# Optimization experiments

Hardware: AMD Instinct MI355X
Metric: run time of the kernel (lower is better)

## Reference

```python
import jax, jax.numpy as jnp
import numpy as np

B, L, D, H, FF, K = 2, 2048, 1024, 16, 4096, 5
HD = D // H
EPS = 1e-5

def _rope_matrix():
    pos = jnp.arange(L, dtype=jnp.float32)
    inv = 1.0 / (10000.0 ** (jnp.arange(0, HD, 2, dtype=jnp.float32) / HD))
    ang = pos[:, None] * inv[None, :]                       # [L, HD//2]
    # buffer layout matches torch: cat([cos, sin], -1) -> [1,1,L,HD]
    return jnp.concatenate([jnp.cos(ang), jnp.sin(ang)], -1)[None, None]

def _alibi():
    i = jnp.arange(L)
    dist = jnp.clip(i[:, None] - i[None, :], 0, None).astype(jnp.float32)
    slopes = 2.0 ** (-(2.0 ** (-(np.log2(H) - 3.0))) * jnp.arange(H, dtype=jnp.float32))
    return slopes[:, None, None] * dist                     # [H,L,L]

def _apply_rope(x, pe):
    # faithful even/odd slicing of the concatenated [cos|sin] buffer
    xe, xo = x[..., ::2], x[..., 1::2]
    c, s = pe[..., ::2], pe[..., 1::2]
    return jnp.concatenate([xe * c - xo * s, xe * s + xo * c], -1)

def _ln(x, g, b):
    m = x.mean(-1, keepdims=True)
    v = ((x - m) ** 2).mean(-1, keepdims=True)
    return (x - m) * jax.lax.rsqrt(v + EPS) * g + b

def _attn(x, wq, bq, wk, bk, wv, bv, wo, bo, pe, alibi):
    q = (x @ wq + bq).reshape(B, L, H, HD).transpose(0, 2, 1, 3)
    k = (x @ wk + bk).reshape(B, L, H, HD).transpose(0, 2, 1, 3)
    v = (x @ wv + bv).reshape(B, L, H, HD).transpose(0, 2, 1, 3)
    q = _apply_rope(q, pe)
    k = _apply_rope(k, pe)
    scores = jnp.einsum('bhqd,bhkd->bhqk', q, k) * (HD ** -0.5) + alibi[None]
    w = jax.nn.softmax(scores, axis=-1)
    o = jnp.einsum('bhqk,bhkd->bhqd', w, v).transpose(0, 2, 1, 3).reshape(B, L, D)
    return o @ wo + bo

def _conv_block(x, g, b, pw1_w, pw1_b, dw_w, dw_b, bn_g, bn_b, pw2_w, pw2_b):
    res = x
    h = _ln(x, g, b)
    h = h @ pw1_w + pw1_b                                   # pointwise 1: [B,L,2D]
    h = h[..., :D] * jax.nn.sigmoid(h[..., D:])             # GLU -> [B,L,D]
    h = h.transpose(0, 2, 1)                                # [B,D,L]
    w = dw_w[:, None, ::-1]                                 # ConvTranspose1d(stride=1,pad=K//2) == corr with flipped kernel
    h = jax.lax.conv_general_dilated(h, w, (1,), [(K // 2, K // 2)],
        dimension_numbers=('NCH', 'OIH', 'NCH'), feature_group_count=D)
    h = h + dw_b[None, :, None]
    h = h * jax.lax.rsqrt(jnp.float32(1.0 + EPS)) * bn_g[None, :, None] + bn_b[None, :, None]  # eval BN
    h = h * jax.nn.relu6(h + 3.0) / 6.0                     # hardswish
    h = h.transpose(0, 2, 1) @ pw2_w + pw2_b                # pointwise 2: [B,L,D]
    return h + res[:, :1, :]                                # Upsample(size=1) residual (nearest -> t=0)

def reference(memory, wq, bq, wk, bk, wv, bv, wo, bo, n1_g, n1_b,
              cln_g, cln_b, pw1_w, pw1_b, dw_w, dw_b, bn_g, bn_b, pw2_w, pw2_b,
              proj_w, proj_b, proj2_w, proj2_b, lin1_w, lin1_b, lin2_w, lin2_b,
              n3_g, n3_b):
    pe = _rope_matrix()
    alibi = _alibi()
    tgt2 = _attn(memory, wq, bq, wk, bk, wv, bv, wo, bo, pe, alibi)
    memory = memory + _ln(tgt2, n1_g, n1_b)
    conv = _conv_block(memory, cln_g, cln_b, pw1_w, pw1_b, dw_w, dw_b,
                       bn_g, bn_b, pw2_w, pw2_b)
    proj = jnp.einsum('bld,lm->bmd', memory, proj_w) + proj_b[:, None]   # Linear over seq axis
    proj = proj @ proj2_w + proj2_b
    memory = proj + conv
    tgt2 = jax.nn.gelu(memory @ lin1_w + lin1_b, approximate=False) @ lin2_w + lin2_b
    return _ln(memory + tgt2, n3_g, n3_b)

def setup_inputs():
    ks = iter(jax.random.split(jax.random.key(0), 48))
    def w(shape, s=0.02):
        return jax.random.normal(next(ks), shape, dtype=jnp.float32) * s
    z = lambda *s: jnp.zeros(s, dtype=jnp.float32)
    o = lambda *s: jnp.ones(s, dtype=jnp.float32)
    return {
        'memory': jax.random.normal(next(ks), (B, L, D), dtype=jnp.float32),
        'wq': w((D, D)), 'bq': z(D), 'wk': w((D, D)), 'bk': z(D),
        'wv': w((D, D)), 'bv': z(D), 'wo': w((D, D)), 'bo': z(D),
        'n1_g': o(D), 'n1_b': z(D),
        'cln_g': o(D), 'cln_b': z(D),
        'pw1_w': w((D, 2 * D)), 'pw1_b': z(2 * D),
        'dw_w': w((D, K), 0.1), 'dw_b': z(D),
        'bn_g': o(D), 'bn_b': z(D),
        'pw2_w': w((D, D)), 'pw2_b': z(D),
        'proj_w': w((L, L)), 'proj_b': z(L),
        'proj2_w': w((D, D)), 'proj2_b': z(D),
        'lin1_w': w((D, FF)), 'lin1_b': z(FF),
        'lin2_w': w((FF, D)), 'lin2_b': z(D),
        'n3_g': o(D), 'n3_b': z(D),
    }
```

## Files before the change

### kernel.cpp

```cpp
#include <hip/hip_runtime.h>
#include <hip/hip_bf16.h>
#include <math.h>

constexpr int Bc = 2, Lc = 2048, Dc = 1024, Hc = 16, HDc = 64, FFc = 4096;
constexpr int NT = Bc * Lc;
constexpr size_t TD = (size_t)NT * Dc;
constexpr size_t MEG = 1024 * 1024;

__device__ __forceinline__ float ldf(const float* p) { return *p; }
__device__ __forceinline__ unsigned short f2b(float f) {
  __hip_bfloat16 h = __float2bfloat16(f);
  return *reinterpret_cast<unsigned short*>(&h);
}

using frag   = __attribute__((ext_vector_type(8))) short;
using f32x4v = __attribute__((ext_vector_type(4))) float;

__device__ __forceinline__ void async16(const unsigned short* g, unsigned short* l) {
  __builtin_amdgcn_global_load_lds(
      (const __attribute__((address_space(1))) unsigned int*)g,
      (__attribute__((address_space(3))) unsigned int*)l, 16, 0, 0);
}

__device__ __forceinline__ float block_sum(float v, float* red) {
  const int lane = threadIdx.x & 63, w = threadIdx.x >> 6;
  #pragma unroll
  for (int o = 32; o > 0; o >>= 1) v += __shfl_down(v, o, 64);
  __syncthreads();
  if (lane == 0) red[w] = v;
  __syncthreads();
  return red[0] + red[1] + red[2] + red[3];
}

__global__ __launch_bounds__(256)
void convert_bf16_kernel(const float* __restrict__ IN, unsigned short* __restrict__ OUT)
{
  const size_t gid = (size_t)blockIdx.x * 256 + threadIdx.x;
  const float4 v = *(const float4*)(IN + gid * 4);
  ushort4 o;
  o.x = f2b(v.x); o.y = f2b(v.y); o.z = f2b(v.z); o.w = f2b(v.w);
  *(ushort4*)(OUT + gid * 4) = o;
}

__global__ __launch_bounds__(256)
void transpose_convert_kernel(const float* __restrict__ IN, unsigned short* __restrict__ OUT,
                              int R, int C, long long sIn, long long sOut)
{
  __shared__ float tile[64][65];
  const int t = threadIdx.x;
  const float* in = IN + (long long)blockIdx.z * sIn;
  unsigned short* out = OUT + (long long)blockIdx.z * sOut;
  const int r0 = blockIdx.y * 64, c0 = blockIdx.x * 64;
  #pragma unroll
  for (int i = 0; i < 4; i++) {
    const int r = (t >> 4) + i * 16, c4 = (t & 15) * 4;
    const float4 v = *(const float4*)(in + (size_t)(r0 + r) * C + c0 + c4);
    tile[r][c4+0] = v.x; tile[r][c4+1] = v.y; tile[r][c4+2] = v.z; tile[r][c4+3] = v.w;
  }
  __syncthreads();
  #pragma unroll
  for (int i = 0; i < 4; i++) {
    const int cc = (t >> 4) + i * 16, rr4 = (t & 15) * 4;
    ushort4 o;
    o.x = f2b(tile[rr4+0][cc]); o.y = f2b(tile[rr4+1][cc]);
    o.z = f2b(tile[rr4+2][cc]); o.w = f2b(tile[rr4+3][cc]);
    *(ushort4*)(out + (size_t)(c0 + cc) * R + r0 + rr4) = o;
  }
}

struct TPack {
  const float* in[10]; unsigned short* out[10];
  int R[10], C[10], tx[10], start[10];
};
__global__ __launch_bounds__(256)
void fused_transpose_kernel(TPack p)
{
  __shared__ float tile[64][65];
  const int bid = blockIdx.x;
  int s = 0;
  #pragma unroll
  for (int i = 1; i < 10; i++) s = (bid >= p.start[i]) ? i : s;
  const float* in = p.in[s];
  unsigned short* out = p.out[s];
  const int R = p.R[s], C = p.C[s];
  const int local = bid - p.start[s];
  const int bx = local % p.tx[s], by = local / p.tx[s];
  const int r0 = by * 64, c0 = bx * 64;
  const int t = threadIdx.x;
  #pragma unroll
  for (int i = 0; i < 4; i++) {
    const int r = (t >> 4) + i * 16, c4 = (t & 15) * 4;
    const float4 v = *(const float4*)(in + (size_t)(r0 + r) * C + c0 + c4);
    tile[r][c4+0] = v.x; tile[r][c4+1] = v.y; tile[r][c4+2] = v.z; tile[r][c4+3] = v.w;
  }
  __syncthreads();
  #pragma unroll
  for (int i = 0; i < 4; i++) {
    const int cc = (t >> 4) + i * 16, rr4 = (t & 15) * 4;
    ushort4 o;
    o.x = f2b(tile[rr4+0][cc]); o.y = f2b(tile[rr4+1][cc]);
    o.z = f2b(tile[rr4+2][cc]); o.w = f2b(tile[rr4+3][cc]);
    *(ushort4*)(out + (size_t)(c0 + cc) * R + r0 + rr4) = o;
  }
}

constexpr int EPI_BIAS = 0, EPI_BIAS_ROW = 1, EPI_GELU = 2, EPI_ADD = 3, EPI_ADDROW0 = 4,
              EPI_QKV = 5;

template<int BM, int EPI, bool OUTBF, bool OUTBOTH>
__global__ __launch_bounds__(256)
void mfma_gemm_kernel(const unsigned short* __restrict__ A, const unsigned short* __restrict__ Bt,
                      const float* __restrict__ bias, const float* __restrict__ bias2,
                      const float* __restrict__ bias3, const float* __restrict__ extra,
                      float* __restrict__ C, unsigned short* __restrict__ Cbf,
                      int M, int N, int K,
                      long long sA, long long sB, long long sC)
{
  constexpr int NTt = (BM == 128) ? 4 : 2;
  __shared__ unsigned short As[2][BM][4][8];
  __shared__ unsigned short Bs[2][128][4][8];
  const int tid = threadIdx.x;
  const int l = tid & 63, w = tid >> 6;
  const int wm = (BM == 128) ? (w & 1) * 64 : 0;
  const int wn = (BM == 128) ? (w >> 1) * 64 : w * 32;
  const int m0 = blockIdx.y * BM, n0 = blockIdx.x * 128;
  const unsigned short* Ap = A + (long long)blockIdx.z * sA;
  const unsigned short* Bp = Bt + (long long)blockIdx.z * sB;

  f32x4v acc[4][NTt];
  #pragma unroll
  for (int mt = 0; mt < 4; mt++)
    #pragma unroll
    for (int nt = 0; nt < NTt; nt++) acc[mt][nt] = {0.f, 0.f, 0.f, 0.f};

  const int c_ = l >> 4, rm = l & 15;
  int rrB[2], ggB[2];
  #pragma unroll
  for (int j = 0; j < 2; j++) {
    const int chunk = w * 128 + j * 64 + l;
    rrB[j] = chunk >> 2;
    ggB[j] = (chunk & 3) ^ ((rrB[j] >> 1) & 3);
  }
  int rrA = 0, ggA = 0;
  if constexpr (BM == 64) {
    const int chunkA = w * 64 + l;
    rrA = chunkA >> 2;
    ggA = (chunkA & 3) ^ ((rrA >> 1) & 3);
  }

  auto stage = [&](int bi, int k0) {
    if constexpr (BM == 128) {
      #pragma unroll
      for (int j = 0; j < 2; j++) {
        async16(Ap + (size_t)(m0 + rrB[j]) * K + k0 + ggB[j] * 8,
                &As[bi][0][0][0] + (size_t)(w * 128 + j * 64) * 8);
        async16(Bp + (size_t)(n0 + rrB[j]) * K + k0 + ggB[j] * 8,
                &Bs[bi][0][0][0] + (size_t)(w * 128 + j * 64) * 8);
      }
    } else {
      async16(Ap + (size_t)(m0 + rrA) * K + k0 + ggA * 8,
              &As[bi][0][0][0] + (size_t)(w * 64) * 8);
      #pragma unroll
      for (int j = 0; j < 2; j++)
        async16(Bp + (size_t)(n0 + rrB[j]) * K + k0 + ggB[j] * 8,
                &Bs[bi][0][0][0] + (size_t)(w * 128 + j * 64) * 8);
    }
  };

  stage(0, 0);
  __syncthreads();
  int cur = 0;
  const int sg = (rm >> 1) & 3;

  for (int k0 = 0; k0 < K; k0 += 32) {
    if (k0 + 32 < K) stage(cur ^ 1, k0 + 32);

    frag af[4], bfr[NTt];
    #pragma unroll
    for (int mt = 0; mt < 4; mt++)
      af[mt] = *(const frag*)&As[cur][wm + mt * 16 + rm][c_ ^ sg][0];
    #pragma unroll
    for (int nt = 0; nt < NTt; nt++)
      bfr[nt] = *(const frag*)&Bs[cur][wn + nt * 16 + rm][c_ ^ sg][0];
    #pragma unroll
    for (int mt = 0; mt < 4; mt++)
      #pragma unroll
      for (int nt = 0; nt < NTt; nt++)
        acc[mt][nt] = __builtin_amdgcn_mfma_f32_16x16x32_bf16(af[mt], bfr[nt], acc[mt][nt], 0, 0, 0);

    __syncthreads();
    cur ^= 1;
  }

  float* Cp = C + (long long)blockIdx.z * sC;
  unsigned short* Cbp = Cbf + (long long)blockIdx.z * sC;
  #pragma unroll
  for (int mt = 0; mt < 4; mt++) {
    #pragma unroll
    for (int nt = 0; nt < NTt; nt++) {
      const int mq = m0 + wm + mt * 16 + c_ * 4;
      const int n  = n0 + wn + nt * 16 + rm;
      if constexpr (EPI == EPI_QKV) {
        const float* bp = (n < 1024) ? bias : ((n < 2048) ? bias2 : bias3);
        const float bv_ = ldf(bp + (n & 1023));
        const float r0 = acc[mt][nt][0] + bv_;
        const float r1 = acc[mt][nt][1] + bv_;
        const float r2 = acc[mt][nt][2] + bv_;
        const float r3 = acc[mt][nt][3] + bv_;
        if (n < 2048) {
          float* dst = Cp + (size_t)(n >> 10) * TD + (size_t)mq * Dc + (n & 1023);
          dst[0] = r0; dst[Dc] = r1; dst[2 * Dc] = r2; dst[3 * Dc] = r3;
        } else {
          ushort4 o;
          o.x = f2b(r0); o.y = f2b(r1); o.z = f2b(r2); o.w = f2b(r3);
          *(ushort4*)(Cbp + (size_t)(mq >> 11) * ((size_t)Lc * Dc)
                      + (size_t)(n - 2048) * Lc + (mq & (Lc - 1))) = o;
        }
      } else {
        #pragma unroll
        for (int i = 0; i < 4; i++) {
          const int m = mq + i;
          float r = acc[mt][nt][i];
          if constexpr (EPI == EPI_BIAS || EPI == EPI_GELU || EPI == EPI_ADD || EPI == EPI_ADDROW0)
            r += ldf(bias + n);
          if constexpr (EPI == EPI_BIAS_ROW) r += ldf(bias + m);
          if constexpr (EPI == EPI_GELU)
            r = 0.5f * r * (1.0f + erff(r * 0.70710678118654752f));
          if constexpr (EPI == EPI_ADD) r += extra[(size_t)m * N + n];
          if constexpr (EPI == EPI_ADDROW0) r += extra[(size_t)(m >> 11) * ((size_t)Lc * Dc) + n];
          if constexpr (OUTBOTH) { Cp[(size_t)m * N + n] = r; Cbp[(size_t)m * N + n] = f2b(r); }
          else if constexpr (OUTBF) Cbp[(size_t)m * N + n] = f2b(r);
          else                      Cp[(size_t)m * N + n] = r;
        }
      }
    }
  }
}

__global__ __launch_bounds__(256)
void pe_fill_kernel(float* __restrict__ pet)
{
  const int gid = blockIdx.x * 256 + threadIdx.x;
  const int l = gid >> 6, t = gid & 63;
  const int j = t & 31;
  const float wj = exp2f(-(float)j * (13.2877123795494f / 32.0f));
  const float ang = (float)l * wj;
  pet[gid] = (t < 32) ? cosf(ang) : sinf(ang);
}

__global__ __launch_bounds__(256)
void rope2_kernel(const float* __restrict__ Qi, const float* __restrict__ Ki,
                  const float* __restrict__ pet,
                  unsigned short* __restrict__ Qo, unsigned short* __restrict__ Ko)
{
  int gid = blockIdx.x * 256 + threadIdx.x;
  const int sel = gid >= NT * Hc;
  if (sel) gid -= NT * Hc;
  const float* X = sel ? Ki : Qi;
  unsigned short* O = sel ? Ko : Qo;
  const int h = gid & (Hc - 1);
  const int token = gid >> 4;
  const int l = token & (Lc - 1);
  const float* p = X + (size_t)token * Dc + h * HDc;
  unsigned short* po = O + (size_t)token * Dc + h * HDc;
  const float* pr = pet + l * 64;
  float x[64], out[64];
  #pragma unroll
  for (int i = 0; i < 16; i++) *(float4*)&x[4*i] = *(const float4*)&p[4*i];
  #pragma unroll
  for (int u = 0; u < 32; u++) {
    const int base = (u < 16) ? (2 * u) : (32 + 2 * (u - 16));
    const float c = pr[base], s = pr[base + 1];
    out[u]      = x[2*u] * c - x[2*u+1] * s;
    out[32 + u] = x[2*u] * s + x[2*u+1] * c;
  }
  #pragma unroll
  for (int i = 0; i < 16; i++) {
    ushort4 o;
    o.x = f2b(out[4*i+0]); o.y = f2b(out[4*i+1]);
    o.z = f2b(out[4*i+2]); o.w = f2b(out[4*i+3]);
    *(ushort4*)&po[4*i] = o;
  }
}

__global__ __launch_bounds__(256)
void flash_attn_mfma_kernel(const unsigned short* __restrict__ Q,
                            const unsigned short* __restrict__ K,
                            const unsigned short* __restrict__ VT,
                            unsigned short* __restrict__ O)
{
  __shared__ unsigned short Qs[64][8][8];
  __shared__ unsigned short Ks[64][8][8];
  __shared__ unsigned short Vt[64][8][8];
  __shared__ unsigned short Ps[64][72];
  const int tid = threadIdx.x;
  const int l = tid & 63, w = tid >> 6;
  const int lg = l >> 4, lm = l & 15;
  const int q0 = blockIdx.x * 64;
  const int bh = blockIdx.y;
  const int b = bh >> 4, h = bh & 15;
  const size_t rowbase = (size_t)b * Lc;
  const size_t vbase = (size_t)b * Lc * Dc;
  const int dbase = h * 64;
  const float sc1 = 0.125f * 1.44269504f;
  const float sl2 = exp2f(-0.5f * (float)h) * 1.44269504f;

  #pragma unroll
  for (int j = 0; j < 2; j++) {
    const int chunk = (w * 2 + j) * 64 + l;
    const int r = chunk >> 3, gsrc = (chunk & 7) ^ (r & 7);
    async16(Q + (rowbase + q0 + r) * Dc + dbase + gsrc * 8,
            &Qs[0][0][0] + (size_t)chunk * 8);
  }
  __syncthreads();
  frag qf[2];
  #pragma unroll
  for (int s = 0; s < 2; s++)
    qf[s] = *(const frag*)&Qs[w * 16 + lm][(s * 4 + lg) ^ (lm & 7)][0];

  float m_i = -3.0e38f, l_i = 0.f;
  f32x4v acc_o[4];
  #pragma unroll
  for (int dt = 0; dt < 4; dt++) acc_o[dt] = {0.f, 0.f, 0.f, 0.f};

  for (int k0 = 0; k0 < Lc; k0 += 64) {
    __syncthreads();
    #pragma unroll
    for (int j = 0; j < 2; j++) {
      const int chunk = (w * 2 + j) * 64 + l;
      const int r = chunk >> 3, gsrc = (chunk & 7) ^ (r & 7);
      async16(K + (rowbase + k0 + r) * Dc + dbase + gsrc * 8,
              &Ks[0][0][0] + (size_t)chunk * 8);
      async16(VT + vbase + (size_t)(dbase + r) * Lc + k0 + gsrc * 8,
              &Vt[0][0][0] + (size_t)chunk * 8);
    }
    __syncthreads();

    f32x4v st[4];
    #pragma unroll
    for (int kt = 0; kt < 4; kt++) st[kt] = {0.f, 0.f, 0.f, 0.f};
    __builtin_amdgcn_s_setprio(1);
    #pragma unroll
    for (int kt = 0; kt < 4; kt++) {
      #pragma unroll
      for (int s = 0; s < 2; s++) {
        frag kf = *(const frag*)&Ks[kt * 16 + lm][(s * 4 + lg) ^ (lm & 7)][0];
        st[kt] = __builtin_amdgcn_mfma_f32_16x16x32_bf16(kf, qf[s], st[kt], 0, 0, 0);
      }
    }
    __builtin_amdgcn_s_setprio(0);

    const float qg = (float)(q0 + w * 16 + lm);
    float sv[4][4], tmax = -3.0e38f;
    #pragma unroll
    for (int kt = 0; kt < 4; kt++)
      #pragma unroll
      for (int i = 0; i < 4; i++) {
        const float kg = (float)(k0 + kt * 16 + lg * 4 + i);
        const float v = st[kt][i] * sc1 + sl2 * fmaxf(qg - kg, 0.0f);
        sv[kt][i] = v; tmax = fmaxf(tmax, v);
      }
    tmax = fmaxf(tmax, __shfl_xor(tmax, 16, 64));
    tmax = fmaxf(tmax, __shfl_xor(tmax, 32, 64));
    if (__any(tmax > m_i)) {
      const float mnew = fmaxf(m_i, tmax);
      const float alpha = exp2f(m_i - mnew);
      m_i = mnew;
      l_i *= alpha;
      float aO[4];
      #pragma unroll
      for (int i = 0; i < 4; i++) aO[i] = __shfl(alpha, lg * 4 + i, 64);
      #pragma unroll
      for (int dt = 0; dt < 4; dt++)
        #pragma unroll
        for (int i = 0; i < 4; i++) acc_o[dt][i] *= aO[i];
    }
    float rsum = 0.f;
    const int qrow = w * 16 + lm;
    #pragma unroll
    for (int kt = 0; kt < 4; kt++) {
      const float p0 = exp2f(sv[kt][0] - m_i), p1 = exp2f(sv[kt][1] - m_i);
      const float p2 = exp2f(sv[kt][2] - m_i), p3 = exp2f(sv[kt][3] - m_i);
      rsum += (p0 + p1) + (p2 + p3);
      ushort4 pk4;
      pk4.x = f2b(p0); pk4.y = f2b(p1); pk4.z = f2b(p2); pk4.w = f2b(p3);
      *(ushort4*)&Ps[qrow][kt * 16 + lg * 4] = pk4;
    }
    rsum += __shfl_xor(rsum, 16, 64);
    rsum += __shfl_xor(rsum, 32, 64);
    l_i += rsum;

    __builtin_amdgcn_s_setprio(1);
    #pragma unroll
    for (int c = 0; c < 2; c++) {
      frag ap = *(const frag*)&Ps[w * 16 + lm][c * 32 + lg * 8];
      #pragma unroll
      for (int dt = 0; dt < 4; dt++) {
        frag bv = *(const frag*)&Vt[dt * 16 + lm][(c * 4 + lg) ^ (lm & 7)][0];
        acc_o[dt] = __builtin_amdgcn_mfma_f32_16x16x32_bf16(ap, bv, acc_o[dt], 0, 0, 0);
      }
    }
    __builtin_amdgcn_s_setprio(0);
  }

  float lO[4];
  #pragma unroll
  for (int i = 0; i < 4; i++) lO[i] = 1.0f / __shfl(l_i, lg * 4 + i, 64);
  #pragma unroll
  for (int dt = 0; dt < 4; dt++)
    #pragma unroll
    for (int i = 0; i < 4; i++)
      Ps[w * 16 + lg * 4 + i][dt * 16 + lm] = f2b(acc_o[dt][i] * lO[i]);
  __syncthreads();
  #pragma unroll
  for (int j = 0; j < 2; j++) {
    const int chunk = (w * 2 + j) * 64 + l;
    const int r = chunk >> 3, g = chunk & 7;
    alignas(16) unsigned short tmp[8];
    #pragma unroll
    for (int t = 0; t < 8; t++) tmp[t] = Ps[r][g * 8 + t];
    *(uint4*)(O + (rowbase + q0 + r) * Dc + dbase + g * 8) = *(uint4*)tmp;
  }
}

__global__ __launch_bounds__(256)
void ln_res_cln_kernel(const float* __restrict__ X, const float* __restrict__ RES,
                       const float* __restrict__ g1, const float* __restrict__ b1,
                       const float* __restrict__ g2, const float* __restrict__ b2,
                       float* __restrict__ OUT1, unsigned short* __restrict__ OUT2)
{
  __shared__ float red4[4];
  const int row = blockIdx.x, tid = threadIdx.x;
  const size_t base = (size_t)row * Dc + tid * 4;
  const float4 xv = *(const float4*)(X + base);
  float s = xv.x + xv.y + xv.z + xv.w;
  s = block_sum(s, red4);
  const float mean = s * (1.0f / Dc);
  const float d0 = xv.x-mean, d1 = xv.y-mean, d2 = xv.z-mean, d3 = xv.w-mean;
  float ss = d0*d0 + d1*d1 + d2*d2 + d3*d3;
  ss = block_sum(ss, red4);
  const float rstd = rsqrtf(ss * (1.0f / Dc) + 1e-5f);
  const int c = tid * 4;
  const float4 rv = *(const float4*)(RES + base);
  float y0 = rv.x + d0*rstd*ldf(g1+c+0) + ldf(b1+c+0);
  float y1 = rv.y + d1*rstd*ldf(g1+c+1) + ldf(b1+c+1);
  float y2 = rv.z + d2*rstd*ldf(g1+c+2) + ldf(b1+c+2);
  float y3 = rv.w + d3*rstd*ldf(g1+c+3) + ldf(b1+c+3);
  *(float4*)(OUT1 + base) = make_float4(y0, y1, y2, y3);
  float s2 = y0 + y1 + y2 + y3;
  s2 = block_sum(s2, red4);
  const float mean2 = s2 * (1.0f / Dc);
  const float e0 = y0-mean2, e1 = y1-mean2, e2 = y2-mean2, e3 = y3-mean2;
  float ss2 = e0*e0 + e1*e1 + e2*e2 + e3*e3;
  ss2 = block_sum(ss2, red4);
  const float rstd2 = rsqrtf(ss2 * (1.0f / Dc) + 1e-5f);
  ushort4 o;
  o.x = f2b(e0*rstd2*ldf(g2+c+0) + ldf(b2+c+0));
  o.y = f2b(e1*rstd2*ldf(g2+c+1) + ldf(b2+c+1));
  o.z = f2b(e2*rstd2*ldf(g2+c+2) + ldf(b2+c+2));
  o.w = f2b(e3*rstd2*ldf(g2+c+3) + ldf(b2+c+3));
  *(ushort4*)(OUT2 + base) = o;
}

__global__ __launch_bounds__(256)
void ln_sum_kernel(const float* __restrict__ X, const float* __restrict__ Y,
                   const float* __restrict__ g, const float* __restrict__ be,
                   float* __restrict__ OUT)
{
  __shared__ float red4[4];
  const int row = blockIdx.x, tid = threadIdx.x;
  const size_t base = (size_t)row * Dc + tid * 4;
  const float4 xv = *(const float4*)(X + base);
  const float4 yv = *(const float4*)(Y + base);
  const float x0 = xv.x+yv.x, x1 = xv.y+yv.y, x2 = xv.z+yv.z, x3 = xv.w+yv.w;
  float s = x0 + x1 + x2 + x3;
  s = block_sum(s, red4);
  const float mean = s * (1.0f / Dc);
  const float d0 = x0-mean, d1 = x1-mean, d2 = x2-mean, d3 = x3-mean;
  float ss = d0*d0 + d1*d1 + d2*d2 + d3*d3;
  ss = block_sum(ss, red4);
  const float rstd = rsqrtf(ss * (1.0f / Dc) + 1e-5f);
  const int c = tid * 4;
  float4 o;
  o.x = d0*rstd*ldf(g+c+0) + ldf(be+c+0);
  o.y = d1*rstd*ldf(g+c+1) + ldf(be+c+1);
  o.z = d2*rstd*ldf(g+c+2) + ldf(be+c+2);
  o.w = d3*rstd*ldf(g+c+3) + ldf(be+c+3);
  *(float4*)(OUT + base) = o;
}

__global__ __launch_bounds__(256)
void glu_kernel(const float* __restrict__ H1, float* __restrict__ HG)
{
  const int gid = blockIdx.x * 256 + threadIdx.x;
  const int t = gid >> 8;
  const int c4 = (gid & 255) * 4;
  const float* p = H1 + (size_t)t * (2 * Dc);
  const float4 a = *(const float4*)(p + c4);
  const float4 gg = *(const float4*)(p + Dc + c4);
  float4 o;
  o.x = a.x / (1.0f + expf(-gg.x));
  o.y = a.y / (1.0f + expf(-gg.y));
  o.z = a.z / (1.0f + expf(-gg.z));
  o.w = a.w / (1.0f + expf(-gg.w));
  *(float4*)(HG + (size_t)t * Dc + c4) = o;
}

__global__ __launch_bounds__(256)
void dwconv_bf16_kernel(const float* __restrict__ HG, const float* __restrict__ w,
                        const float* __restrict__ wb, const float* __restrict__ gn,
                        const float* __restrict__ bb, unsigned short* __restrict__ OUT)
{
  const int gid = blockIdx.x * 256 + threadIdx.x;
  const int d = gid & (Dc - 1);
  const int l = (gid >> 10) & (Lc - 1);
  const int b = gid >> 21;
  const size_t rowb = (size_t)b * Lc;
  float acc = ldf(wb + d);
  #pragma unroll
  for (int s = 0; s < 5; s++) {
    const int lp = l + 2 - s;
    if (lp >= 0 && lp < Lc)
      acc += ldf(w + d * 5 + s) * HG[((rowb + lp) << 10) + d];
  }
  const float rs = rsqrtf(1.0f + 1e-5f);
  const float t = acc * rs * ldf(gn + d) + ldf(bb + d);
  OUT[gid] = f2b(t * fminf(fmaxf(t + 3.0f, 0.0f), 6.0f) * (1.0f / 6.0f));
}

extern "C" void kernel_launch(void* const* d_in, const int* in_sizes, int n_in,
                              void* d_out, int out_size, void* d_ws, size_t ws_size,
                              hipStream_t stream) {
  (void)in_sizes; (void)n_in; (void)out_size; (void)ws_size;
  const float* mem    = (const float*)d_in[0];
  const float* wq     = (const float*)d_in[1];
  const float* bq     = (const float*)d_in[2];
  const float* wk     = (const float*)d_in[3];
  const float* bk     = (const float*)d_in[4];
  const float* wv     = (const float*)d_in[5];
  const float* bv     = (const float*)d_in[6];
  const float* wo     = (const float*)d_in[7];
  const float* bo     = (const float*)d_in[8];
  const float* n1g    = (const float*)d_in[9];
  const float* n1b    = (const float*)d_in[10];
  const float* clng   = (const float*)d_in[11];
  const float* clnb   = (const float*)d_in[12];
  const float* pw1w   = (const float*)d_in[13];
  const float* pw1b   = (const float*)d_in[14];
  const float* dww    = (const float*)d_in[15];
  const float* dwb    = (const float*)d_in[16];
  const float* bng    = (const float*)d_in[17];
  const float* bnb    = (const float*)d_in[18];
  const float* pw2w   = (const float*)d_in[19];
  const float* pw2b   = (const float*)d_in[20];
  const float* projw  = (const float*)d_in[21];
  const float* projb  = (const float*)d_in[22];
  const float* proj2w = (const float*)d_in[23];
  const float* proj2b = (const float*)d_in[24];
  const float* lin1w  = (const float*)d_in[25];
  const float* lin1b  = (const float*)d_in[26];
  const float* lin2w  = (const float*)d_in[27];
  const float* lin2b  = (const float*)d_in[28];
  const float* n3g    = (const float*)d_in[29];
  const float* n3b    = (const float*)d_in[30];
  float* out = (float*)d_out;

  char* base = (char*)d_ws;
  float* qb   = (float*)base;
  float* kb   = qb + TD;
  float* big1 = kb + TD;
  float* big2 = big1 + TD;
  float* ob   = big2 + TD;
  unsigned short* abf  = (unsigned short*)(base + 5 * TD * 4);
  unsigned short* qbf  = abf + TD;
  unsigned short* kbf  = qbf + TD;
  unsigned short* vtb  = kbf + TD;
  unsigned short* m1T  = vtb + TD;
  unsigned short* ffbbf= m1T + TD;
  unsigned short* wt   = ffbbf + 4 * TD;
  unsigned short* wqT    = wt;
  unsigned short* wkT    = wqT + MEG;
  unsigned short* wvT    = wkT + MEG;
  unsigned short* woT    = wvT + MEG;
  unsigned short* pw1T   = woT + MEG;
  unsigned short* pw2T   = pw1T + 2*MEG;
  unsigned short* proj2T = pw2T + MEG;
  unsigned short* projwT = proj2T + MEG;
  unsigned short* lin1T  = projwT + 4*MEG;
  unsigned short* lin2T  = lin1T + 4*MEG;
  float* pet = (float*)(lin2T + 4*MEG);

  const dim3 blk(256);
  const long long LD = (long long)Lc * Dc;

  TPack tp;
  const float* tin[10]  = {wq, wk, wv, wo, pw1w, pw2w, proj2w, projw, lin1w, lin2w};
  unsigned short* tout[10] = {wqT, wkT, wvT, woT, pw1T, pw2T, proj2T, projwT, lin1T, lin2T};
  const int tR[10] = {1024,1024,1024,1024,1024,1024,1024,2048,1024,4096};
  const int tC[10] = {1024,1024,1024,1024,2048,1024,1024,2048,4096,1024};
  int startAcc = 0;
  for (int i = 0; i < 10; i++) {
    tp.in[i] = tin[i]; tp.out[i] = tout[i];
    tp.R[i] = tR[i]; tp.C[i] = tC[i]; tp.tx[i] = tC[i] / 64;
    tp.start[i] = startAcc;
    startAcc += (tR[i] / 64) * (tC[i] / 64);
  }
  fused_transpose_kernel<<<dim3(startAcc), blk, 0, stream>>>(tp);
  pe_fill_kernel<<<dim3(Lc * 64 / 256), blk, 0, stream>>>(pet);

  convert_bf16_kernel<<<dim3((unsigned)(TD/1024)),blk,0,stream>>>(mem, abf);
  mfma_gemm_kernel<128,EPI_QKV,false,false><<<dim3(24,32,1),blk,0,stream>>>(
      abf, wqT, bq, bk, bv, nullptr, qb, vtb, NT, 3*Dc, Dc, 0, 0, 0);
  rope2_kernel<<<dim3(2*NT*Hc/256),blk,0,stream>>>(qb, kb, pet, qbf, kbf);
  flash_attn_mfma_kernel<<<dim3(Lc/64, Bc*Hc),blk,0,stream>>>(qbf,kbf,vtb,abf);
  mfma_gemm_kernel<64,EPI_BIAS,false,false><<<dim3(8,64,1),blk,0,stream>>>(
      abf,woT,bo,nullptr,nullptr,nullptr,qb,nullptr,NT,Dc,Dc,0,0,0);
  ln_res_cln_kernel<<<dim3(NT),blk,0,stream>>>(qb, mem, n1g, n1b, clng, clnb, kb, abf);

  mfma_gemm_kernel<128,EPI_BIAS,false,false><<<dim3(16,32,1),blk,0,stream>>>(
      abf,pw1T,pw1b,nullptr,nullptr,nullptr,big1,nullptr,NT,2*Dc,Dc,0,0,0);
  glu_kernel<<<dim3((unsigned)(TD/4/256)),blk,0,stream>>>(big1, ob);
  dwconv_bf16_kernel<<<dim3((unsigned)(TD/256)),blk,0,stream>>>(ob, dww, dwb, bng, bnb, abf);
  mfma_gemm_kernel<64,EPI_ADDROW0,false,false><<<dim3(8,64,1),blk,0,stream>>>(
      abf,pw2T,pw2b,nullptr,nullptr,kb,big2,nullptr,NT,Dc,Dc,0,0,0);

  transpose_convert_kernel<<<dim3(16,32,2),blk,0,stream>>>(kb, m1T, 2048, 1024, LD, LD);
  mfma_gemm_kernel<64,EPI_BIAS_ROW,true,false><<<dim3(8,32,2),blk,0,stream>>>(
      projwT,m1T,projb,nullptr,nullptr,nullptr,nullptr,abf,Lc,Dc,Lc,0,LD,LD);
  mfma_gemm_kernel<64,EPI_ADD,false,true><<<dim3(8,64,1),blk,0,stream>>>(
      abf,proj2T,proj2b,nullptr,nullptr,big2,big1,qbf,NT,Dc,Dc,0,0,0);

  mfma_gemm_kernel<128,EPI_GELU,true,false><<<dim3(32,32,1),blk,0,stream>>>(
      qbf,lin1T,lin1b,nullptr,nullptr,nullptr,nullptr,ffbbf,NT,FFc,Dc,0,0,0);
  mfma_gemm_kernel<64,EPI_BIAS,false,false><<<dim3(8,64,1),blk,0,stream>>>(
      ffbbf,lin2T,lin2b,nullptr,nullptr,nullptr,ob,nullptr,NT,Dc,FFc,0,0,0);

  ln_sum_kernel<<<dim3(NT),blk,0,stream>>>(big1, ob, n3g, n3b, out);
}
```

Baseline: 649.7 us.

## Double-buffer K/V tiles, fold Q scale into RoPE, skip negligible attention tiles

The attention kernel now prefetches the next K/V tile into a second LDS buffer while computing the current one, and uses a single barrier per iteration instead of two. The softmax scale is folded into Q inside the RoPE kernel. ALiBi bias evaluation is specialised for tiles that are fully past, on the diagonal, or fully future. A warp-uniform check skips the exp and PV MFMA work for tiles whose scores sit more than 27 log2 units below the running max. That skip drops tiny contributions and so slightly changes the numerics, and the second buffer doubles the LDS used for K/V, which could reduce occupancy.

```diff
diff --git a/kernel.cpp b/kernel.cpp
--- a/kernel.cpp
+++ b/kernel.cpp
@@ -258,6 +258,7 @@
   if (sel) gid -= NT * Hc;
   const float* X = sel ? Ki : Qi;
   unsigned short* O = sel ? Ko : Qo;
+  const float scl = sel ? 1.0f : 0.125f * 1.44269504f;
   const int h = gid & (Hc - 1);
   const int token = gid >> 4;
   const int l = token & (Lc - 1);
@@ -271,8 +272,8 @@
   for (int u = 0; u < 32; u++) {
     const int base = (u < 16) ? (2 * u) : (32 + 2 * (u - 16));
     const float c = pr[base], s = pr[base + 1];
-    out[u]      = x[2*u] * c - x[2*u+1] * s;
-    out[32 + u] = x[2*u] * s + x[2*u+1] * c;
+    out[u]      = (x[2*u] * c - x[2*u+1] * s) * scl;
+    out[32 + u] = (x[2*u] * s + x[2*u+1] * c) * scl;
   }
   #pragma unroll
   for (int i = 0; i < 16; i++) {
@@ -290,8 +291,8 @@
                             unsigned short* __restrict__ O)
 {
   __shared__ unsigned short Qs[64][8][8];
-  __shared__ unsigned short Ks[64][8][8];
-  __shared__ unsigned short Vt[64][8][8];
+  __shared__ unsigned short Ks[2][64][8][8];
+  __shared__ unsigned short Vt[2][64][8][8];
   __shared__ unsigned short Ps[64][72];
   const int tid = threadIdx.x;
   const int l = tid & 63, w = tid >> 6;
@@ -302,8 +303,19 @@
   const size_t rowbase = (size_t)b * Lc;
   const size_t vbase = (size_t)b * Lc * Dc;
   const int dbase = h * 64;
-  const float sc1 = 0.125f * 1.44269504f;
   const float sl2 = exp2f(-0.5f * (float)h) * 1.44269504f;
+
+  auto stageKV = [&](int bi, int k0s) {
+    #pragma unroll
+    for (int j = 0; j < 2; j++) {
+      const int chunk = (w * 2 + j) * 64 + l;
+      const int r = chunk >> 3, gsrc = (chunk & 7) ^ (r & 7);
+      async16(K + (rowbase + k0s + r) * Dc + dbase + gsrc * 8,
+              &Ks[bi][0][0][0] + (size_t)chunk * 8);
+      async16(VT + vbase + (size_t)(dbase + r) * Lc + k0s + gsrc * 8,
+              &Vt[bi][0][0][0] + (size_t)chunk * 8);
+    }
+  };
 
   #pragma unroll
   for (int j = 0; j < 2; j++) {
@@ -312,29 +324,28 @@
     async16(Q + (rowbase + q0 + r) * Dc + dbase + gsrc * 8,
             &Qs[0][0][0] + (size_t)chunk * 8);
   }
+  stageKV(0, 0);
   __syncthreads();
   frag qf[2];
   #pragma unroll
   for (int s = 0; s < 2; s++)
     qf[s] = *(const frag*)&Qs[w * 16 + lm][(s * 4 + lg) ^ (lm & 7)][0];
 
+  const float qg = (float)(q0 + w * 16 + lm);
+  float koff[4][4];
+  #pragma unroll
+  for (int kt = 0; kt < 4; kt++)
+    #pragma unroll
+    for (int i = 0; i < 4; i++) koff[kt][i] = (float)(kt * 16 + lg * 4 + i);
+
   float m_i = -3.0e38f, l_i = 0.f;
   f32x4v acc_o[4];
   #pragma unroll
   for (int dt = 0; dt < 4; dt++) acc_o[dt] = {0.f, 0.f, 0.f, 0.f};
 
+  int cur = 0;
   for (int k0 = 0; k0 < Lc; k0 += 64) {
-    __syncthreads();
-    #pragma unroll
-    for (int j = 0; j < 2; j++) {
-      const int chunk = (w * 2 + j) * 64 + l;
-      const int r = chunk >> 3, gsrc = (chunk & 7) ^ (r & 7);
-      async16(K + (rowbase + k0 + r) * Dc + dbase + gsrc * 8,
-              &Ks[0][0][0] + (size_t)chunk * 8);
-      async16(VT + vbase + (size_t)(dbase + r) * Lc + k0 + gsrc * 8,
-              &Vt[0][0][0] + (size_t)chunk * 8);
-    }
-    __syncthreads();
+    if (k0 + 64 < Lc) stageKV(cur ^ 1, k0 + 64);
 
     f32x4v st[4];
     #pragma unroll
@@ -344,63 +355,86 @@
     for (int kt = 0; kt < 4; kt++) {
       #pragma unroll
       for (int s = 0; s < 2; s++) {
-        frag kf = *(const frag*)&Ks[kt * 16 + lm][(s * 4 + lg) ^ (lm & 7)][0];
+        frag kf = *(const frag*)&Ks[cur][kt * 16 + lm][(s * 4 + lg) ^ (lm & 7)][0];
         st[kt] = __builtin_amdgcn_mfma_f32_16x16x32_bf16(kf, qf[s], st[kt], 0, 0, 0);
       }
     }
     __builtin_amdgcn_s_setprio(0);
 
-    const float qg = (float)(q0 + w * 16 + lm);
+    const float qk0 = qg - (float)k0;
     float sv[4][4], tmax = -3.0e38f;
-    #pragma unroll
-    for (int kt = 0; kt < 4; kt++)
-      #pragma unroll
-      for (int i = 0; i < 4; i++) {
-        const float kg = (float)(k0 + kt * 16 + lg * 4 + i);
-        const float v = st[kt][i] * sc1 + sl2 * fmaxf(qg - kg, 0.0f);
-        sv[kt][i] = v; tmax = fmaxf(tmax, v);
-      }
+    if (k0 + 64 <= q0) {
+      #pragma unroll
+      for (int kt = 0; kt < 4; kt++)
+        #pragma unroll
+        for (int i = 0; i < 4; i++) {
+          const float v = fmaf(sl2, qk0 - koff[kt][i], st[kt][i]);
+          sv[kt][i] = v; tmax = fmaxf(tmax, v);
+        }
+    } else if (k0 <= q0) {
+      #pragma unroll
+      for (int kt = 0; kt < 4; kt++)
+        #pragma unroll
+        for (int i = 0; i < 4; i++) {
+          const float v = fmaf(sl2, fmaxf(qk0 - koff[kt][i], 0.f), st[kt][i]);
+          sv[kt][i] = v; tmax = fmaxf(tmax, v);
+        }
+    } else {
+      #pragma unroll
+      for (int kt = 0; kt < 4; kt++)
+        #pragma unroll
+        for (int i = 0; i < 4; i++) {
+          const float v = st[kt][i];
+          sv[kt][i] = v; tmax = fmaxf(tmax, v);
+        }
+    }
     tmax = fmaxf(tmax, __shfl_xor(tmax, 16, 64));
     tmax = fmaxf(tmax, __shfl_xor(tmax, 32, 64));
-    if (__any(tmax > m_i)) {
-      const float mnew = fmaxf(m_i, tmax);
-      const float alpha = exp2f(m_i - mnew);
-      m_i = mnew;
-      l_i *= alpha;
-      float aO[4];
-      #pragma unroll
-      for (int i = 0; i < 4; i++) aO[i] = __shfl(alpha, lg * 4 + i, 64);
-      #pragma unroll
-      for (int dt = 0; dt < 4; dt++)
+
+    if (!__all(tmax < m_i - 27.0f)) {
+      if (__any(tmax > m_i)) {
+        const float mnew = fmaxf(m_i, tmax);
+        const float alpha = exp2f(m_i - mnew);
+        m_i = mnew;
+        l_i *= alpha;
+        float aO[4];
         #pragma unroll
-        for (int i = 0; i < 4; i++) acc_o[dt][i] *= aO[i];
+        for (int i = 0; i < 4; i++) aO[i] = __shfl(alpha, lg * 4 + i, 64);
+        #pragma unroll
+        for (int dt = 0; dt < 4; dt++)
+          #pragma unroll
+          for (int i = 0; i < 4; i++) acc_o[dt][i] *= aO[i];
+      }
+      float rsum = 0.f;
+      const int qrow = w * 16 + lm;
+      #pragma unroll
+      for (int kt = 0; kt < 4; kt++) {
+        const float p0 = exp2f(sv[kt][0] - m_i), p1 = exp2f(sv[kt][1] - m_i);
+        const float p2 = exp2f(sv[kt][2] - m_i), p3 = exp2f(sv[kt][3] - m_i);
+        rsum += (p0 + p1) + (p2 + p3);
+        ushort4 pk4;
+        pk4.x = f2b(p0); pk4.y = f2b(p1); pk4.z = f2b(p2); pk4.w = f2b(p3);
+        *(ushort4*)&Ps[qrow][kt * 16 + lg * 4] = pk4;
+      }
+      rsum += __shfl_xor(rsum, 16, 64);
+      rsum += __shfl_xor(rsum, 32, 64);
+      l_i += rsum;
+
+      __builtin_amdgcn_s_setprio(1);
+      #pragma unroll
+      for (int c = 0; c < 2; c++) {
+        frag ap = *(const frag*)&Ps[w * 16 + lm][c * 32 + lg * 8];
+        #pragma unroll
+        for (int dt = 0; dt < 4; dt++) {
+          frag bv = *(const frag*)&Vt[cur][dt * 16 + lm][(c * 4 + lg) ^ (lm & 7)][0];
+          acc_o[dt] = __builtin_amdgcn_mfma_f32_16x16x32_bf16(ap, bv, acc_o[dt], 0, 0, 0);
+        }
+      }
+      __builtin_amdgcn_s_setprio(0);
     }
-    float rsum = 0.f;
-    const int qrow = w * 16 + lm;
-    #pragma unroll
-    for (int kt = 0; kt < 4; kt++) {
-      const float p0 = exp2f(sv[kt][0] - m_i), p1 = exp2f(sv[kt][1] - m_i);
-      const float p2 = exp2f(sv[kt][2] - m_i), p3 = exp2f(sv[kt][3] - m_i);
-      rsum += (p0 + p1) + (p2 + p3);
-      ushort4 pk4;
-      pk4.x = f2b(p0); pk4.y = f2b(p1); pk4.z = f2b(p2); pk4.w = f2b(p3);
-      *(ushort4*)&Ps[qrow][kt * 16 + lg * 4] = pk4;
-    }
-    rsum += __shfl_xor(rsum, 16, 64);
-    rsum += __shfl_xor(rsum, 32, 64);
-    l_i += rsum;
-
-    __builtin_amdgcn_s_setprio(1);
-    #pragma unroll
-    for (int c = 0; c < 2; c++) {
-      frag ap = *(const frag*)&Ps[w * 16 + lm][c * 32 + lg * 8];
-      #pragma unroll
-      for (int dt = 0; dt < 4; dt++) {
-        frag bv = *(const frag*)&Vt[dt * 16 + lm][(c * 4 + lg) ^ (lm & 7)][0];
-        acc_o[dt] = __builtin_amdgcn_mfma_f32_16x16x32_bf16(ap, bv, acc_o[dt], 0, 0, 0);
-      }
-    }
-    __builtin_amdgcn_s_setprio(0);
+
+    __syncthreads();
+    cur ^= 1;
   }
 
   float lO[4];
```

Measured after the change: 653.6 us. No clear change (+0.6%).
